# Kernel tuning notes

Measured on AMD Instinct MI355X. Metric: run time of the kernel, lower is better.

The kernel has to match this reference:

```python
import jax, jax.numpy as jnp
import numpy as np

NUM_LAYERS = 24
LN_EPS = 1e-5


def setup_inputs() -> dict:
    key = jax.random.key(0)
    ks = jax.random.split(key, 8)
    B, S = 256, 8192
    x = jax.random.uniform(ks[0], (B, S, 5), dtype=jnp.float32)
    # per-layer LayerNorm(4) params (torch default init: weight=1, bias=0; use
    # randomized values so the gather is non-trivial)
    ln_w = 1.0 + 0.1 * jax.random.normal(ks[1], (NUM_LAYERS, 4), dtype=jnp.float32)
    ln_b = 0.1 * jax.random.normal(ks[2], (NUM_LAYERS, 4), dtype=jnp.float32)
    # MLP 5 -> 64 -> 32 -> 1 (dropout inactive in eval mode)
    W1 = jax.random.normal(ks[3], (64, 5), dtype=jnp.float32) / np.sqrt(5)
    b1 = jnp.zeros((64,), dtype=jnp.float32)
    W2 = jax.random.normal(ks[4], (32, 64), dtype=jnp.float32) / np.sqrt(64)
    b2 = jnp.zeros((32,), dtype=jnp.float32)
    W3 = jax.random.normal(ks[5], (1, 32), dtype=jnp.float32) / np.sqrt(32)
    b3 = jnp.zeros((1,), dtype=jnp.float32)
    return {"x": x, "ln_w": ln_w, "ln_b": ln_b, "W1": W1, "b1": b1,
            "W2": W2, "b2": b2, "W3": W3, "b3": b3}


def reference(x, ln_w, ln_b, W1, b1, W2, b2, W3, b3):
    B, S, _ = x.shape
    x_flat = x.reshape(-1, 5)                      # [N, 5]
    layer_pos = x_flat[:, -1]                      # [N]
    layer_ids = jnp.clip((layer_pos * NUM_LAYERS).astype(jnp.int32), 0, NUM_LAYERS - 1)
    feats = x_flat[:, :4]                          # [N, 4]
    # vectorized per-token LayerNorm: gather per-token gamma/beta by layer id
    mean = jnp.mean(feats, axis=-1, keepdims=True)
    var = jnp.mean(jnp.square(feats - mean), axis=-1, keepdims=True)  # biased, as torch LN
    normed = (feats - mean) * jax.lax.rsqrt(var + LN_EPS)
    normed = normed * ln_w[layer_ids] + ln_b[layer_ids]               # [N, 4]
    x_norm = jnp.concatenate([normed, layer_pos[:, None]], axis=1)    # [N, 5]
    h = jax.nn.relu(x_norm @ W1.T + b1)            # [N, 64]
    h = jax.nn.relu(h @ W2.T + b2)                 # [N, 32]
    scores = h @ W3.T + b3                         # [N, 1]
    return scores.reshape(B, S)
```

## Files before the change

### kernel.cpp

```cpp
#include <hip/hip_runtime.h>
#include <stdint.h>

#define NUM_LAYERS 24
#define LN_EPS 1e-5f
#define N_ROWS (256 * 8192)
#define NUM_BLOCKS 2048

typedef __attribute__((ext_vector_type(4)))  uint32_t u32x4;
typedef __attribute__((ext_vector_type(16))) float    f32x16;
typedef __attribute__((ext_vector_type(2)))  float    f32x2;
typedef __attribute__((ext_vector_type(2)))  __fp16   h16x2;

__device__ __forceinline__ uint32_t pk_f16_rtz(float lo, float hi) {
    h16x2 v = __builtin_amdgcn_cvt_pkrtz(lo, hi);
    uint32_t u; __builtin_memcpy(&u, &v, 4);
    return u;
}
__device__ __forceinline__ uint32_t pk_f16_rne(float lo, float hi) {
    __fp16 a = (__fp16)lo, b = (__fp16)hi;
    uint16_t ua, ub;
    __builtin_memcpy(&ua, &a, 2); __builtin_memcpy(&ub, &b, 2);
    return (uint32_t)ua | ((uint32_t)ub << 16);
}
__device__ __forceinline__ uint32_t pk_relu_f16(uint32_t d) {
    h16x2 v; __builtin_memcpy(&v, &d, 4);
    h16x2 z = {(__fp16)0.0f, (__fp16)0.0f};
    v = __builtin_elementwise_max(v, z);
    uint32_t u; __builtin_memcpy(&u, &v, 4);
    return u;
}

__device__ __forceinline__ u32x4 make_frag(uint32_t d0, uint32_t d1,
                                           uint32_t d2, uint32_t d3) {
    u32x4 f; f.x = d0; f.y = d1; f.z = d2; f.w = d3;
    return f;
}

__device__ __forceinline__ void mfma_l1(f32x16& d0, f32x16& d1,
                                        f32x16& d2, f32x16& d3,
                                        const u32x4& a0, const u32x4& a1,
                                        const u32x4& b0, const u32x4& b1) {
    asm("s_nop 2\n\t"
        "v_mfma_f32_32x32x16_f16 %0, %4, %6, 0\n\t"
        "v_mfma_f32_32x32x16_f16 %1, %5, %6, 0\n\t"
        "v_mfma_f32_32x32x16_f16 %2, %4, %7, 0\n\t"
        "v_mfma_f32_32x32x16_f16 %3, %5, %7, 0"
        : "=&v"(d0), "=&v"(d1), "=&v"(d2), "=&v"(d3)
        : "v"(a0), "v"(a1), "v"(b0), "v"(b1));
}
__device__ __forceinline__ void mfma_l2(f32x16& c0, f32x16& c1, const f32x16& cinit,
                                        const u32x4& w0, const u32x4& w1,
                                        const u32x4& w2, const u32x4& w3,
                                        const u32x4& h00, const u32x4& h01,
                                        const u32x4& h02, const u32x4& h03,
                                        const u32x4& h10, const u32x4& h11,
                                        const u32x4& h12, const u32x4& h13) {
    asm("s_nop 2\n\t"
        "v_mfma_f32_32x32x16_f16 %0, %3, %7, %2\n\t"
        "v_mfma_f32_32x32x16_f16 %1, %3, %11, %2\n\t"
        "v_mfma_f32_32x32x16_f16 %0, %4, %8, %0\n\t"
        "v_mfma_f32_32x32x16_f16 %1, %4, %12, %1\n\t"
        "v_mfma_f32_32x32x16_f16 %0, %5, %9, %0\n\t"
        "v_mfma_f32_32x32x16_f16 %1, %5, %13, %1\n\t"
        "v_mfma_f32_32x32x16_f16 %0, %6, %10, %0\n\t"
        "v_mfma_f32_32x32x16_f16 %1, %6, %14, %1"
        : "=&v"(c0), "=&v"(c1)
        : "v"(cinit), "v"(w0), "v"(w1), "v"(w2), "v"(w3),
          "v"(h00), "v"(h01), "v"(h02), "v"(h03),
          "v"(h10), "v"(h11), "v"(h12), "v"(h13));
}
__device__ __forceinline__ void mfma_fence2(f32x16& c0, f32x16& c1) {
    asm volatile("s_nop 7\n\ts_nop 7\n\ts_nop 7" : "+v"(c0), "+v"(c1));
}
__device__ __forceinline__ void mfma_fence4(f32x16& c0, f32x16& c1,
                                            f32x16& c2, f32x16& c3) {
    asm volatile("s_nop 7\n\ts_nop 7\n\ts_nop 7"
                 : "+v"(c0), "+v"(c1), "+v"(c2), "+v"(c3));
}

__device__ __forceinline__ int sigma_k(int p) {
    int hh = (p >> 2) & 1;
    int base = (p & 31) - 4 * hh;
    int r = (base & 3) + 4 * (base >> 3);
    return 32 * (p >> 5) + 16 * (r >> 3) + 8 * hh + (r & 7);
}

__global__ __launch_bounds__(256, 2) void router_mfma(
    const float* __restrict__ x,
    const float* __restrict__ ln_w,
    const float* __restrict__ ln_b,
    const float* __restrict__ W1,
    const float* __restrict__ b1,
    const float* __restrict__ W2,
    const float* __restrict__ b2,
    const float* __restrict__ W3,
    const float* __restrict__ b3,
    float* __restrict__ out)
{
    __shared__ uint32_t s_a1[2 * 64 * 4];
    __shared__ uint32_t s_w2[4 * 64 * 4];
    __shared__ float    s_w3[8 * 64 * 2];
    __shared__ float    s_b2[8 * 64 * 2];
    __shared__ float    s_ln[8 * NUM_LAYERS];

    const int t = threadIdx.x;

    if (t < 8 * NUM_LAYERS) {
        const int q = t & 7, lid = t >> 3;
        s_ln[q * NUM_LAYERS + lid] =
            (q < 4) ? ln_w[lid * 4 + q] : ln_b[lid * 4 + (q - 4)];
    }
    if (t < 128) {
        const int mt = t >> 6, ln = t & 63;
        const int n32l = ln & 31, hl = ln >> 5;
        uint32_t d0 = 0, d1 = 0, d2 = 0;
        if (!hl) {
            const int k = sigma_k(mt * 32 + n32l);
            d0 = pk_f16_rne(W1[k * 5 + 0], W1[k * 5 + 1]);
            d1 = pk_f16_rne(W1[k * 5 + 2], W1[k * 5 + 3]);
            d2 = pk_f16_rne(W1[k * 5 + 4], b1[k]);
        }
        uint32_t* p = &s_a1[(mt * 64 + ln) * 4];
        p[0] = d0; p[1] = d1; p[2] = d2; p[3] = 0;
    }
    {
        const int kt = t >> 6, ln = t & 63;
        const int n32l = ln & 31, hl = ln >> 5;
        const float* wp = W2 + n32l * 64 + kt * 16 + hl * 8;
        const float4 lo = *(const float4*)(wp);
        const float4 hi = *(const float4*)(wp + 4);
        uint32_t* p = &s_w2[(kt * 64 + ln) * 4];
        p[0] = pk_f16_rne(lo.x, lo.y);
        p[1] = pk_f16_rne(lo.z, lo.w);
        p[2] = pk_f16_rne(hi.x, hi.y);
        p[3] = pk_f16_rne(hi.z, hi.w);
    }
#pragma unroll
    for (int e = t; e < 512; e += 256) {
        const int r2 = e >> 6, ln = e & 63;
        const int hl = ln >> 5;
        const int n = ((2 * r2) & 3) + 8 * (r2 >> 1) + 4 * hl;
        s_w3[e * 2 + 0] = W3[n];
        s_w3[e * 2 + 1] = W3[n + 1];
        s_b2[e * 2 + 0] = b2[n];
        s_b2[e * 2 + 1] = b2[n + 1];
    }
    __syncthreads();

    const int lane = t & 63;
    const int wid  = t >> 6;
    const int h    = lane >> 5;

    u32x4 a1f[2], w2f[4];
#pragma unroll
    for (int mt = 0; mt < 2; ++mt)
        a1f[mt] = *(const u32x4*)&s_a1[(mt * 64 + lane) * 4];
#pragma unroll
    for (int kt = 0; kt < 4; ++kt)
        w2f[kt] = *(const u32x4*)&s_w2[(kt * 64 + lane) * 4];

    f32x16 c2init;
    f32x2 w3p[8];
#pragma unroll
    for (int r2 = 0; r2 < 8; ++r2) {
        w3p[r2] = *(const f32x2*)&s_w3[(r2 * 64 + lane) * 2];
        const f32x2 bp = *(const f32x2*)&s_b2[(r2 * 64 + lane) * 2];
        c2init[2 * r2]     = bp.x;
        c2init[2 * r2 + 1] = bp.y;
    }
    const float b3v = b3[0];
    const f32x2 z2 = {0.0f, 0.0f};

    const int w = blockIdx.x * 4 + wid;
    const size_t rowBase = (size_t)w * 256;

    float4 cv[4];
    float  cl[4];
#pragma unroll
    for (int g = 0; g < 4; ++g) {
        const float* p = x + (rowBase + 64 * g + lane) * 5;
        cv[g] = *(const float4*)p;
        cl[g] = p[4];
    }

    u32x4 bft[4][2];
#pragma unroll
    for (int g = 0; g < 4; ++g) {
        int lid = (int)(cl[g] * (float)NUM_LAYERS);
        lid = lid < 0 ? 0 : (lid > NUM_LAYERS - 1 ? NUM_LAYERS - 1 : lid);

        const float m  = (cv[g].x + cv[g].y + cv[g].z + cv[g].w) * 0.25f;
        const float d0 = cv[g].x - m, d1 = cv[g].y - m,
                    d2 = cv[g].z - m, d3 = cv[g].w - m;
        const float var = (d0 * d0 + d1 * d1 + d2 * d2 + d3 * d3) * 0.25f;
        const float r   = rsqrtf(var + LN_EPS);

        const float xn0 = fmaf(d0, r * s_ln[0 * 24 + lid], s_ln[4 * 24 + lid]);
        const float xn1 = fmaf(d1, r * s_ln[1 * 24 + lid], s_ln[5 * 24 + lid]);
        const float xn2 = fmaf(d2, r * s_ln[2 * 24 + lid], s_ln[6 * 24 + lid]);
        const float xn3 = fmaf(d3, r * s_ln[3 * 24 + lid], s_ln[7 * 24 + lid]);

        const uint32_t e0 = pk_f16_rtz(xn0, xn1);
        const uint32_t e1 = pk_f16_rtz(xn2, xn3);
        const uint32_t e2 = pk_f16_rtz(cl[g], 1.0f);
        const uint32_t x0 = __shfl_xor((int)e0, 32, 64);
        const uint32_t x1 = __shfl_xor((int)e1, 32, 64);
        const uint32_t x2 = __shfl_xor((int)e2, 32, 64);

        bft[g][0] = make_frag(e0, e1, e2, 0u);
        bft[g][1] = make_frag(x0, x1, x2, 0u);
    }

#pragma unroll
    for (int g = 0; g < 4; ++g) {
        const size_t gbase = rowBase + 64 * g;

        f32x16 c1a0, c1b0, c1a1, c1b1;
        mfma_l1(c1a0, c1b0, c1a1, c1b1, a1f[0], a1f[1], bft[g][0], bft[g][1]);
        mfma_fence4(c1a0, c1b0, c1a1, c1b1);

        u32x4 h1f0[4], h1f1[4];
#pragma unroll
        for (int kt = 0; kt < 4; ++kt) {
            const f32x16& c1 = (kt < 2) ? c1a0 : c1b0;
            const int roff = 8 * (kt & 1);
            uint32_t dw[4];
#pragma unroll
            for (int d = 0; d < 4; ++d)
                dw[d] = pk_relu_f16(
                    pk_f16_rtz(c1[roff + 2 * d], c1[roff + 2 * d + 1]));
            h1f0[kt] = make_frag(dw[0], dw[1], dw[2], dw[3]);
        }
#pragma unroll
        for (int kt = 0; kt < 4; ++kt) {
            const f32x16& c1 = (kt < 2) ? c1a1 : c1b1;
            const int roff = 8 * (kt & 1);
            uint32_t dw[4];
#pragma unroll
            for (int d = 0; d < 4; ++d)
                dw[d] = pk_relu_f16(
                    pk_f16_rtz(c1[roff + 2 * d], c1[roff + 2 * d + 1]));
            h1f1[kt] = make_frag(dw[0], dw[1], dw[2], dw[3]);
        }

        f32x16 c2_0, c2_1;
        mfma_l2(c2_0, c2_1, c2init,
                w2f[0], w2f[1], w2f[2], w2f[3],
                h1f0[0], h1f0[1], h1f0[2], h1f0[3],
                h1f1[0], h1f1[1], h1f1[2], h1f1[3]);
        mfma_fence2(c2_0, c2_1);

        f32x2 acc0 = z2, acc1 = z2;
#pragma unroll
        for (int r2 = 0; r2 < 8; ++r2) {
            f32x2 v0 = {c2_0[2 * r2], c2_0[2 * r2 + 1]};
            f32x2 v1 = {c2_1[2 * r2], c2_1[2 * r2 + 1]};
            v0 = __builtin_elementwise_max(v0, z2);
            v1 = __builtin_elementwise_max(v1, z2);
            acc0 = v0 * w3p[r2] + acc0;
            acc1 = v1 * w3p[r2] + acc1;
        }
        float q0 = acc0.x + acc0.y;
        float q1 = acc1.x + acc1.y;
        q0 += __shfl_xor(q0, 32, 64);
        q1 += __shfl_xor(q1, 32, 64);

        out[gbase + lane] = (h ? q1 : q0) + b3v;
    }
}

extern "C" void kernel_launch(void* const* d_in, const int* in_sizes, int n_in,
                              void* d_out, int out_size, void* d_ws, size_t ws_size,
                              hipStream_t stream) {
    const float* x    = (const float*)d_in[0];
    const float* ln_w = (const float*)d_in[1];
    const float* ln_b = (const float*)d_in[2];
    const float* W1   = (const float*)d_in[3];
    const float* b1   = (const float*)d_in[4];
    const float* W2   = (const float*)d_in[5];
    const float* b2   = (const float*)d_in[6];
    const float* W3   = (const float*)d_in[7];
    const float* b3   = (const float*)d_in[8];
    float* out = (float*)d_out;

    router_mfma<<<NUM_BLOCKS, 256, 0, stream>>>(x, ln_w, ln_b, W1, b1, W2, b2,
                                                W3, b3, out);
}
```

Baseline: 106.6 us.

## Cut register pressure to double occupancy by splitting layer-1 MFMAs and streaming W3/b2

Raises launch bounds from 2 to 4 blocks per CU. To fit in fewer VGPRs, the layer-1 MFMAs are split into two halves, each converted to fp16 before the next one runs, and the per-group fragment preparation is merged into the compute loop. The b2/W3 values now come from an interleaved shared-memory array inside the epilogue instead of being held in registers, with b2 added after the MFMA rather than used as its initial accumulator. This trades more LDS reads and less MFMA batching for higher occupancy, which is meant to hide memory latency.

```diff
diff --git a/kernel.cpp b/kernel.cpp
--- a/kernel.cpp
+++ b/kernel.cpp
@@ -37,45 +37,37 @@
 }
 
 __device__ __forceinline__ void mfma_l1(f32x16& d0, f32x16& d1,
-                                        f32x16& d2, f32x16& d3,
                                         const u32x4& a0, const u32x4& a1,
-                                        const u32x4& b0, const u32x4& b1) {
+                                        const u32x4& b) {
     asm("s_nop 2\n\t"
-        "v_mfma_f32_32x32x16_f16 %0, %4, %6, 0\n\t"
-        "v_mfma_f32_32x32x16_f16 %1, %5, %6, 0\n\t"
-        "v_mfma_f32_32x32x16_f16 %2, %4, %7, 0\n\t"
-        "v_mfma_f32_32x32x16_f16 %3, %5, %7, 0"
-        : "=&v"(d0), "=&v"(d1), "=&v"(d2), "=&v"(d3)
-        : "v"(a0), "v"(a1), "v"(b0), "v"(b1));
-}
-__device__ __forceinline__ void mfma_l2(f32x16& c0, f32x16& c1, const f32x16& cinit,
-                                        const u32x4& w0, const u32x4& w1,
-                                        const u32x4& w2, const u32x4& w3,
-                                        const u32x4& h00, const u32x4& h01,
-                                        const u32x4& h02, const u32x4& h03,
-                                        const u32x4& h10, const u32x4& h11,
-                                        const u32x4& h12, const u32x4& h13) {
+        "v_mfma_f32_32x32x16_f16 %0, %2, %4, 0\n\t"
+        "v_mfma_f32_32x32x16_f16 %1, %3, %4, 0"
+        : "=&v"(d0), "=&v"(d1)
+        : "v"(a0), "v"(a1), "v"(b));
+}
+__device__ __forceinline__ void mfma_l2z(f32x16& c0, f32x16& c1,
+                                         const u32x4& w0, const u32x4& w1,
+                                         const u32x4& w2, const u32x4& w3,
+                                         const u32x4& h00, const u32x4& h01,
+                                         const u32x4& h02, const u32x4& h03,
+                                         const u32x4& h10, const u32x4& h11,
+                                         const u32x4& h12, const u32x4& h13) {
     asm("s_nop 2\n\t"
-        "v_mfma_f32_32x32x16_f16 %0, %3, %7, %2\n\t"
-        "v_mfma_f32_32x32x16_f16 %1, %3, %11, %2\n\t"
+        "v_mfma_f32_32x32x16_f16 %0, %2, %6, 0\n\t"
+        "v_mfma_f32_32x32x16_f16 %1, %2, %10, 0\n\t"
+        "v_mfma_f32_32x32x16_f16 %0, %3, %7, %0\n\t"
+        "v_mfma_f32_32x32x16_f16 %1, %3, %11, %1\n\t"
         "v_mfma_f32_32x32x16_f16 %0, %4, %8, %0\n\t"
         "v_mfma_f32_32x32x16_f16 %1, %4, %12, %1\n\t"
         "v_mfma_f32_32x32x16_f16 %0, %5, %9, %0\n\t"
-        "v_mfma_f32_32x32x16_f16 %1, %5, %13, %1\n\t"
-        "v_mfma_f32_32x32x16_f16 %0, %6, %10, %0\n\t"
-        "v_mfma_f32_32x32x16_f16 %1, %6, %14, %1"
+        "v_mfma_f32_32x32x16_f16 %1, %5, %13, %1"
         : "=&v"(c0), "=&v"(c1)
-        : "v"(cinit), "v"(w0), "v"(w1), "v"(w2), "v"(w3),
+        : "v"(w0), "v"(w1), "v"(w2), "v"(w3),
           "v"(h00), "v"(h01), "v"(h02), "v"(h03),
           "v"(h10), "v"(h11), "v"(h12), "v"(h13));
 }
 __device__ __forceinline__ void mfma_fence2(f32x16& c0, f32x16& c1) {
     asm volatile("s_nop 7\n\ts_nop 7\n\ts_nop 7" : "+v"(c0), "+v"(c1));
-}
-__device__ __forceinline__ void mfma_fence4(f32x16& c0, f32x16& c1,
-                                            f32x16& c2, f32x16& c3) {
-    asm volatile("s_nop 7\n\ts_nop 7\n\ts_nop 7"
-                 : "+v"(c0), "+v"(c1), "+v"(c2), "+v"(c3));
 }
 
 __device__ __forceinline__ int sigma_k(int p) {
@@ -85,7 +77,7 @@
     return 32 * (p >> 5) + 16 * (r >> 3) + 8 * hh + (r & 7);
 }
 
-__global__ __launch_bounds__(256, 2) void router_mfma(
+__global__ __launch_bounds__(256, 4) void router_mfma(
     const float* __restrict__ x,
     const float* __restrict__ ln_w,
     const float* __restrict__ ln_b,
@@ -99,8 +91,7 @@
 {
     __shared__ uint32_t s_a1[2 * 64 * 4];
     __shared__ uint32_t s_w2[4 * 64 * 4];
-    __shared__ float    s_w3[8 * 64 * 2];
-    __shared__ float    s_b2[8 * 64 * 2];
+    __shared__ float    s_wb[8 * 64 * 4];
     __shared__ float    s_ln[8 * NUM_LAYERS];
 
     const int t = threadIdx.x;
@@ -140,10 +131,9 @@
         const int r2 = e >> 6, ln = e & 63;
         const int hl = ln >> 5;
         const int n = ((2 * r2) & 3) + 8 * (r2 >> 1) + 4 * hl;
-        s_w3[e * 2 + 0] = W3[n];
-        s_w3[e * 2 + 1] = W3[n + 1];
-        s_b2[e * 2 + 0] = b2[n];
-        s_b2[e * 2 + 1] = b2[n + 1];
+        float* p = &s_wb[e * 4];
+        p[0] = W3[n]; p[1] = W3[n + 1];
+        p[2] = b2[n]; p[3] = b2[n + 1];
     }
     __syncthreads();
 
@@ -159,15 +149,6 @@
     for (int kt = 0; kt < 4; ++kt)
         w2f[kt] = *(const u32x4*)&s_w2[(kt * 64 + lane) * 4];
 
-    f32x16 c2init;
-    f32x2 w3p[8];
-#pragma unroll
-    for (int r2 = 0; r2 < 8; ++r2) {
-        w3p[r2] = *(const f32x2*)&s_w3[(r2 * 64 + lane) * 2];
-        const f32x2 bp = *(const f32x2*)&s_b2[(r2 * 64 + lane) * 2];
-        c2init[2 * r2]     = bp.x;
-        c2init[2 * r2 + 1] = bp.y;
-    }
     const float b3v = b3[0];
     const f32x2 z2 = {0.0f, 0.0f};
 
@@ -183,9 +164,10 @@
         cl[g] = p[4];
     }
 
-    u32x4 bft[4][2];
 #pragma unroll
     for (int g = 0; g < 4; ++g) {
+        const size_t gbase = rowBase + 64 * g;
+
         int lid = (int)(cl[g] * (float)NUM_LAYERS);
         lid = lid < 0 ? 0 : (lid > NUM_LAYERS - 1 ? NUM_LAYERS - 1 : lid);
 
@@ -207,58 +189,61 @@
         const uint32_t x1 = __shfl_xor((int)e1, 32, 64);
         const uint32_t x2 = __shfl_xor((int)e2, 32, 64);
 
-        bft[g][0] = make_frag(e0, e1, e2, 0u);
-        bft[g][1] = make_frag(x0, x1, x2, 0u);
-    }
-
-#pragma unroll
-    for (int g = 0; g < 4; ++g) {
-        const size_t gbase = rowBase + 64 * g;
-
-        f32x16 c1a0, c1b0, c1a1, c1b1;
-        mfma_l1(c1a0, c1b0, c1a1, c1b1, a1f[0], a1f[1], bft[g][0], bft[g][1]);
-        mfma_fence4(c1a0, c1b0, c1a1, c1b1);
+        const u32x4 bf_t0 = make_frag(e0, e1, e2, 0u);
+        const u32x4 bf_t1 = make_frag(x0, x1, x2, 0u);
 
         u32x4 h1f0[4], h1f1[4];
-#pragma unroll
-        for (int kt = 0; kt < 4; ++kt) {
-            const f32x16& c1 = (kt < 2) ? c1a0 : c1b0;
-            const int roff = 8 * (kt & 1);
-            uint32_t dw[4];
-#pragma unroll
-            for (int d = 0; d < 4; ++d)
-                dw[d] = pk_relu_f16(
-                    pk_f16_rtz(c1[roff + 2 * d], c1[roff + 2 * d + 1]));
-            h1f0[kt] = make_frag(dw[0], dw[1], dw[2], dw[3]);
-        }
-#pragma unroll
-        for (int kt = 0; kt < 4; ++kt) {
-            const f32x16& c1 = (kt < 2) ? c1a1 : c1b1;
-            const int roff = 8 * (kt & 1);
-            uint32_t dw[4];
-#pragma unroll
-            for (int d = 0; d < 4; ++d)
-                dw[d] = pk_relu_f16(
-                    pk_f16_rtz(c1[roff + 2 * d], c1[roff + 2 * d + 1]));
-            h1f1[kt] = make_frag(dw[0], dw[1], dw[2], dw[3]);
+        {
+            f32x16 c1a, c1b;
+            mfma_l1(c1a, c1b, a1f[0], a1f[1], bf_t0);
+            mfma_fence2(c1a, c1b);
+#pragma unroll
+            for (int kt = 0; kt < 4; ++kt) {
+                const f32x16& c1 = (kt < 2) ? c1a : c1b;
+                const int roff = 8 * (kt & 1);
+                uint32_t dw[4];
+#pragma unroll
+                for (int d = 0; d < 4; ++d)
+                    dw[d] = pk_relu_f16(
+                        pk_f16_rtz(c1[roff + 2 * d], c1[roff + 2 * d + 1]));
+                h1f0[kt] = make_frag(dw[0], dw[1], dw[2], dw[3]);
+            }
+        }
+        {
+            f32x16 c1a, c1b;
+            mfma_l1(c1a, c1b, a1f[0], a1f[1], bf_t1);
+            mfma_fence2(c1a, c1b);
+#pragma unroll
+            for (int kt = 0; kt < 4; ++kt) {
+                const f32x16& c1 = (kt < 2) ? c1a : c1b;
+                const int roff = 8 * (kt & 1);
+                uint32_t dw[4];
+#pragma unroll
+                for (int d = 0; d < 4; ++d)
+                    dw[d] = pk_relu_f16(
+                        pk_f16_rtz(c1[roff + 2 * d], c1[roff + 2 * d + 1]));
+                h1f1[kt] = make_frag(dw[0], dw[1], dw[2], dw[3]);
+            }
         }
 
         f32x16 c2_0, c2_1;
-        mfma_l2(c2_0, c2_1, c2init,
-                w2f[0], w2f[1], w2f[2], w2f[3],
-                h1f0[0], h1f0[1], h1f0[2], h1f0[3],
-                h1f1[0], h1f1[1], h1f1[2], h1f1[3]);
+        mfma_l2z(c2_0, c2_1,
+                 w2f[0], w2f[1], w2f[2], w2f[3],
+                 h1f0[0], h1f0[1], h1f0[2], h1f0[3],
+                 h1f1[0], h1f1[1], h1f1[2], h1f1[3]);
         mfma_fence2(c2_0, c2_1);
 
         f32x2 acc0 = z2, acc1 = z2;
 #pragma unroll
         for (int r2 = 0; r2 < 8; ++r2) {
-            f32x2 v0 = {c2_0[2 * r2], c2_0[2 * r2 + 1]};
-            f32x2 v1 = {c2_1[2 * r2], c2_1[2 * r2 + 1]};
+            const float4 wb = *(const float4*)&s_wb[(r2 * 64 + lane) * 4];
+            f32x2 v0 = {c2_0[2 * r2] + wb.z, c2_0[2 * r2 + 1] + wb.w};
+            f32x2 v1 = {c2_1[2 * r2] + wb.z, c2_1[2 * r2 + 1] + wb.w};
             v0 = __builtin_elementwise_max(v0, z2);
             v1 = __builtin_elementwise_max(v1, z2);
-            acc0 = v0 * w3p[r2] + acc0;
-            acc1 = v1 * w3p[r2] + acc1;
+            const f32x2 w3v = {wb.x, wb.y};
+            acc0 = v0 * w3v + acc0;
+            acc1 = v1 * w3v + acc1;
         }
         float q0 = acc0.x + acc0.y;
         float q1 = acc1.x + acc1.y;
```

Measured after the change: 104.6 us. Within noise of the previous version (-1.9%).
